# Optimization experiments

Hardware: AMD Instinct MI355X
Metric: run time of the kernel (lower is better)

## Reference

```python
import jax, jax.numpy as jnp
import numpy as np

B = 4096          # graphs in batch
NODES = 256       # nodes per graph
N = B * NODES     # total nodes
D = 64            # latent_dim
H = 128           # hidden
NEG = jnp.float32(np.finfo(np.float32).min)


def setup_inputs() -> dict:
    key = jax.random.key(0)
    ks = jax.random.split(key, 5)
    embed = jax.random.normal(ks[0], (N, D), jnp.float32)
    graph_embed = jax.random.normal(ks[1], (B, D), jnp.float32)
    prefix_sum = (jnp.arange(B, dtype=jnp.int32) + 1) * NODES  # cumulative node counts
    banned = jax.random.randint(ks[2], (N,), 0, 2) == 1        # per-node banned-action mask
    W1 = jax.random.normal(ks[3], (2 * D, H), jnp.float32) * 0.05
    b1 = jnp.zeros((H,), jnp.float32)
    W2 = jax.random.normal(ks[4], (H, 1), jnp.float32) * 0.05
    b2 = jnp.zeros((1,), jnp.float32)
    return dict(embed=embed, graph_embed=graph_embed, prefix_sum=prefix_sum,
                banned=banned, W1=W1, b1=b1, W2=W2, b2=b2)


def reference(embed, graph_embed, prefix_sum, banned, W1, b1, W2, b2):
    n = embed.shape[0]
    b = prefix_sum.shape[0]
    # node -> graph id (replaces rep_idx python loop in rep_global_embed)
    seg_ids = jnp.searchsorted(prefix_sum, jnp.arange(n, dtype=prefix_sum.dtype), side='right')
    g_rep = graph_embed[seg_ids]                                 # [N, D] gathered graph embed
    # linear_1 -> relu -> linear_out
    h = jax.nn.relu(jnp.concatenate([embed, g_rep], axis=1) @ W1 + b1)  # [N, H]
    raw_pred = h @ W2 + b2                                       # [N, 1]
    # greedy_actions: index_fill banned with float32 min, then per-graph argmax (jmax)
    q = jnp.where(banned, NEG, raw_pred[:, 0])                   # [N]
    seg_max = jax.ops.segment_max(q, seg_ids, num_segments=b)    # [B]
    is_max = q == seg_max[seg_ids]
    cand = jnp.where(is_max, jnp.arange(n), n)
    gidx = jax.ops.segment_min(cand, seg_ids, num_segments=b)    # global argmax per graph
    starts = jnp.concatenate([jnp.zeros((1,), prefix_sum.dtype), prefix_sum[:-1]])
    actions = gidx.astype(prefix_sum.dtype) - starts             # local (per-graph) action ids
    values = q[gidx]
    return actions, values, raw_pred
```

## Files before the change

kernel.cpp:

```cpp
#include <hip/hip_runtime.h>

#define NEGF (-3.402823466e+38f)
constexpr int BG = 4096;

typedef __attribute__((ext_vector_type(8))) short short8;
typedef __attribute__((ext_vector_type(4))) float f32x4;

constexpr int WT_STRIDE = 72;
constexpr int WT_ELEMS  = 128 * WT_STRIDE;

__device__ __forceinline__ void split_bf16(float a, short& hi, short& lo) {
    const unsigned u = __float_as_uint(a);
    hi = (short)(u >> 16);
    const float lof = a - __uint_as_float(u & 0xffff0000u);
    lo = (short)(__float_as_uint(lof) >> 16);
}

__global__ __launch_bounds__(256) void k_init(const float* __restrict__ W1,
                                              unsigned short* __restrict__ wt) {
    const int e = blockIdx.x * 256 + threadIdx.x;
    const int k = e >> 7, j = e & 127;
    short hi, lo;
    split_bf16(W1[e], hi, lo);
    wt[j * WT_STRIDE + k] = (unsigned short)hi;
    wt[WT_ELEMS + j * WT_STRIDE + k] = (unsigned short)lo;
}

__global__ __launch_bounds__(256, 2) void k_fused(
    const float* __restrict__ embed, const float* __restrict__ ge,
    const float* __restrict__ W1, const float* __restrict__ b1,
    const float* __restrict__ W2, const float* __restrict__ b2,
    const int* __restrict__ banned, const unsigned short* __restrict__ wt,
    float* __restrict__ out) {

    __shared__ __align__(16) unsigned short sW[2 * WT_ELEMS];
    __shared__ float s_ge[64];
    __shared__ float s_gp[2][128];
    __shared__ float s_gt[128];
    __shared__ float s_w2[128];
    __shared__ float s_raw[256];
    __shared__ float s_rv[4];
    __shared__ int   s_ri[4];

    const int t = threadIdx.x;
    const int lane = t & 63;
    const int w = t >> 6;
    const int quad = lane >> 4;
    const int l15 = lane & 15;
    const int g = blockIdx.x;

    const float* ebase = embed + ((size_t)g * 256 + (size_t)w * 64 + l15) * 64;
    f32x4 araw[4][2][2];
#pragma unroll
    for (int mt = 0; mt < 4; ++mt)
#pragma unroll
        for (int kc = 0; kc < 2; ++kc) {
            const float* p = ebase + mt * 1024 + kc * 32 + quad * 8;
            araw[mt][kc][0] = *(const f32x4*)p;
            araw[mt][kc][1] = *(const f32x4*)(p + 4);
        }

    {
        const uint4* src = (const uint4*)wt;
        uint4* dst = (uint4*)sW;
#pragma unroll
        for (int i = 0; i < 9; ++i) dst[i * 256 + t] = src[i * 256 + t];
    }
    if (t < 64) s_ge[t] = ge[g * 64 + t];
    if (t >= 64 && t < 192) s_w2[t - 64] = W2[t - 64];
    __syncthreads();

    {
        const int j = t & 127, h = t >> 7;
        float s = 0.f;
        const float* wb = W1 + (64 + h * 32) * 128 + j;
#pragma unroll
        for (int k = 0; k < 32; ++k) s = fmaf(s_ge[h * 32 + k], wb[k * 128], s);
        s_gp[h][j] = s;
    }
    __syncthreads();
    if (t < 128) s_gt[t] = s_gp[0][t] + s_gp[1][t] + b1[t];

    short8 ahi[4][2], alo[4][2];
#pragma unroll
    for (int mt = 0; mt < 4; ++mt)
#pragma unroll
        for (int kc = 0; kc < 2; ++kc)
#pragma unroll
            for (int i = 0; i < 8; ++i) {
                const float a = (i < 4) ? araw[mt][kc][0][i] : araw[mt][kc][1][i - 4];
                short hi, lo;
                split_bf16(a, hi, lo);
                ahi[mt][kc][i] = hi;
                alo[mt][kc][i] = lo;
            }

    f32x4 acc[4][8];
#pragma unroll
    for (int mt = 0; mt < 4; ++mt)
#pragma unroll
        for (int nt = 0; nt < 8; ++nt) acc[mt][nt] = f32x4{0.f, 0.f, 0.f, 0.f};

#pragma unroll
    for (int nt = 0; nt < 8; ++nt) {
        const unsigned short* rowp = sW + (nt * 16 + l15) * WT_STRIDE + quad * 8;
        const short8 bhi0 = *(const short8*)rowp;
        const short8 bhi1 = *(const short8*)(rowp + 32);
        const short8 blo0 = *(const short8*)(rowp + WT_ELEMS);
        const short8 blo1 = *(const short8*)(rowp + WT_ELEMS + 32);
#pragma unroll
        for (int mt = 0; mt < 4; ++mt) {
            f32x4 c = acc[mt][nt];
            c = __builtin_amdgcn_mfma_f32_16x16x32_bf16(ahi[mt][0], bhi0, c, 0, 0, 0);
            c = __builtin_amdgcn_mfma_f32_16x16x32_bf16(ahi[mt][1], bhi1, c, 0, 0, 0);
            c = __builtin_amdgcn_mfma_f32_16x16x32_bf16(alo[mt][0], bhi0, c, 0, 0, 0);
            c = __builtin_amdgcn_mfma_f32_16x16x32_bf16(alo[mt][1], bhi1, c, 0, 0, 0);
            c = __builtin_amdgcn_mfma_f32_16x16x32_bf16(ahi[mt][0], blo0, c, 0, 0, 0);
            c = __builtin_amdgcn_mfma_f32_16x16x32_bf16(ahi[mt][1], blo1, c, 0, 0, 0);
            acc[mt][nt] = c;
        }
    }

    __syncthreads();

    float gt8[8], w28[8];
#pragma unroll
    for (int nt = 0; nt < 8; ++nt) {
        gt8[nt] = s_gt[nt * 16 + l15];
        w28[nt] = s_w2[nt * 16 + l15];
    }
#pragma unroll
    for (int mt = 0; mt < 4; ++mt) {
        float pr[4] = {0.f, 0.f, 0.f, 0.f};
#pragma unroll
        for (int nt = 0; nt < 8; ++nt)
#pragma unroll
            for (int r = 0; r < 4; ++r)
                pr[r] = fmaf(fmaxf(acc[mt][nt][r] + gt8[nt], 0.f), w28[nt], pr[r]);
#pragma unroll
        for (int m = 1; m <= 8; m <<= 1)
#pragma unroll
            for (int r = 0; r < 4; ++r)
                pr[r] += __shfl_xor(pr[r], m, 64);
        if (l15 == 0) {
            float* dst = s_raw + w * 64 + mt * 16 + quad * 4;
            dst[0] = pr[0]; dst[1] = pr[1]; dst[2] = pr[2]; dst[3] = pr[3];
        }
    }
    __syncthreads();

    const float rp = s_raw[t] + b2[0];
    out[2 * BG + (size_t)g * 256 + t] = rp;
    float q = banned[(size_t)g * 256 + t] ? NEGF : rp;
    int idx = t;
#pragma unroll
    for (int off = 32; off >= 1; off >>= 1) {
        const float qv = __shfl_down(q, off, 64);
        const int iv = __shfl_down(idx, off, 64);
        if (qv > q || (qv == q && iv < idx)) { q = qv; idx = iv; }
    }
    if (lane == 0) { s_rv[w] = q; s_ri[w] = idx; }
    __syncthreads();
    if (t == 0) {
#pragma unroll
        for (int i = 1; i < 4; ++i)
            if (s_rv[i] > q || (s_rv[i] == q && s_ri[i] < idx)) { q = s_rv[i]; idx = s_ri[i]; }
        out[g] = (float)idx;
        out[BG + g] = q;
    }
}

extern "C" void kernel_launch(void* const* d_in, const int* in_sizes, int n_in,
                              void* d_out, int out_size, void* d_ws, size_t ws_size,
                              hipStream_t stream) {
    const float* embed  = (const float*)d_in[0];
    const float* gembed = (const float*)d_in[1];
    const int* banned   = (const int*)d_in[3];
    const float* W1     = (const float*)d_in[4];
    const float* b1     = (const float*)d_in[5];
    const float* W2     = (const float*)d_in[6];
    const float* b2     = (const float*)d_in[7];
    float* out = (float*)d_out;
    unsigned short* wt = (unsigned short*)d_ws;

    k_init<<<32, 256, 0, stream>>>(W1, wt);
    k_fused<<<BG, 256, 0, stream>>>(embed, gembed, W1, b1, W2, b2, banned, wt, out);
}
```

Measured before the change: 464.0 us.

## Split each graph over two blocks with precomputed graph term and atomic argmax

Moves the per-graph graph_embed·W1 projection into a separate kernel, then processes each graph with two 128-node blocks at higher occupancy. The per-graph argmax is combined across blocks with a 64-bit ordered-key atomicMax, and a final kernel decodes action and value. This aims to improve latency hiding and shrink per-block register pressure, but doubles the per-block weight copies into shared memory and adds two kernel launches plus a global round trip.

```diff
diff --git a/kernel.cpp b/kernel.cpp
--- a/kernel.cpp
+++ b/kernel.cpp
@@ -26,19 +26,31 @@
     wt[WT_ELEMS + j * WT_STRIDE + k] = (unsigned short)lo;
 }
 
-__global__ __launch_bounds__(256, 2) void k_fused(
-    const float* __restrict__ embed, const float* __restrict__ ge,
-    const float* __restrict__ W1, const float* __restrict__ b1,
-    const float* __restrict__ W2, const float* __restrict__ b2,
-    const int* __restrict__ banned, const unsigned short* __restrict__ wt,
-    float* __restrict__ out) {
+__global__ __launch_bounds__(128) void k_gterm(const float* __restrict__ ge,
+                                               const float* __restrict__ W1,
+                                               const float* __restrict__ b1,
+                                               float* __restrict__ gterm,
+                                               unsigned long long* __restrict__ keys) {
+    const int g = blockIdx.x, j = threadIdx.x;
+    if (j == 0) keys[g] = 0ull;
+    __shared__ float sg[64];
+    if (j < 64) sg[j] = ge[g * 64 + j];
+    __syncthreads();
+    float s = b1[j];
+    const float* w = W1 + 64 * 128 + j;
+#pragma unroll
+    for (int k = 0; k < 64; ++k) s = fmaf(sg[k], w[k * 128], s);
+    gterm[g * 128 + j] = s;
+}
+
+__global__ __launch_bounds__(256, 3) void k_main(
+    const float* __restrict__ embed, const float* __restrict__ gterm,
+    const unsigned short* __restrict__ wt, const float* __restrict__ W2,
+    const float* __restrict__ b2, const int* __restrict__ banned,
+    float* __restrict__ raw, unsigned long long* __restrict__ keys) {
 
     __shared__ __align__(16) unsigned short sW[2 * WT_ELEMS];
-    __shared__ float s_ge[64];
-    __shared__ float s_gp[2][128];
-    __shared__ float s_gt[128];
-    __shared__ float s_w2[128];
-    __shared__ float s_raw[256];
+    __shared__ float s_raw[128];
     __shared__ float s_rv[4];
     __shared__ int   s_ri[4];
 
@@ -47,18 +59,20 @@
     const int w = t >> 6;
     const int quad = lane >> 4;
     const int l15 = lane & 15;
-    const int g = blockIdx.x;
-
-    const float* ebase = embed + ((size_t)g * 256 + (size_t)w * 64 + l15) * 64;
-    f32x4 araw[4][2][2];
-#pragma unroll
-    for (int mt = 0; mt < 4; ++mt)
-#pragma unroll
-        for (int kc = 0; kc < 2; ++kc) {
-            const float* p = ebase + mt * 1024 + kc * 32 + quad * 8;
-            araw[mt][kc][0] = *(const f32x4*)p;
-            araw[mt][kc][1] = *(const f32x4*)(p + 4);
-        }
+    const int blk = blockIdx.x;
+    const int g = blk >> 1;
+    const int half = blk & 1;
+    const size_t node0 = (size_t)g * 256 + half * 128 + w * 32;
+
+    f32x4 araw[2][4];
+#pragma unroll
+    for (int mt = 0; mt < 2; ++mt) {
+        const float* p = embed + (node0 + mt * 16 + l15) * 64 + quad * 8;
+        araw[mt][0] = *(const f32x4*)p;
+        araw[mt][1] = *(const f32x4*)(p + 4);
+        araw[mt][2] = *(const f32x4*)(p + 32);
+        araw[mt][3] = *(const f32x4*)(p + 36);
+    }
 
     {
         const uint4* src = (const uint4*)wt;
@@ -66,38 +80,25 @@
 #pragma unroll
         for (int i = 0; i < 9; ++i) dst[i * 256 + t] = src[i * 256 + t];
     }
-    if (t < 64) s_ge[t] = ge[g * 64 + t];
-    if (t >= 64 && t < 192) s_w2[t - 64] = W2[t - 64];
-    __syncthreads();
-
-    {
-        const int j = t & 127, h = t >> 7;
-        float s = 0.f;
-        const float* wb = W1 + (64 + h * 32) * 128 + j;
-#pragma unroll
-        for (int k = 0; k < 32; ++k) s = fmaf(s_ge[h * 32 + k], wb[k * 128], s);
-        s_gp[h][j] = s;
-    }
-    __syncthreads();
-    if (t < 128) s_gt[t] = s_gp[0][t] + s_gp[1][t] + b1[t];
-
-    short8 ahi[4][2], alo[4][2];
-#pragma unroll
-    for (int mt = 0; mt < 4; ++mt)
+
+    short8 ahi[2][2], alo[2][2];
+#pragma unroll
+    for (int mt = 0; mt < 2; ++mt)
 #pragma unroll
         for (int kc = 0; kc < 2; ++kc)
 #pragma unroll
             for (int i = 0; i < 8; ++i) {
-                const float a = (i < 4) ? araw[mt][kc][0][i] : araw[mt][kc][1][i - 4];
+                const float a = (i < 4) ? araw[mt][kc * 2][i] : araw[mt][kc * 2 + 1][i - 4];
                 short hi, lo;
                 split_bf16(a, hi, lo);
                 ahi[mt][kc][i] = hi;
                 alo[mt][kc][i] = lo;
             }
-
-    f32x4 acc[4][8];
-#pragma unroll
-    for (int mt = 0; mt < 4; ++mt)
+    __syncthreads();
+
+    f32x4 acc[2][8];
+#pragma unroll
+    for (int mt = 0; mt < 2; ++mt)
 #pragma unroll
         for (int nt = 0; nt < 8; ++nt) acc[mt][nt] = f32x4{0.f, 0.f, 0.f, 0.f};
 
@@ -109,7 +110,7 @@
         const short8 blo0 = *(const short8*)(rowp + WT_ELEMS);
         const short8 blo1 = *(const short8*)(rowp + WT_ELEMS + 32);
 #pragma unroll
-        for (int mt = 0; mt < 4; ++mt) {
+        for (int mt = 0; mt < 2; ++mt) {
             f32x4 c = acc[mt][nt];
             c = __builtin_amdgcn_mfma_f32_16x16x32_bf16(ahi[mt][0], bhi0, c, 0, 0, 0);
             c = __builtin_amdgcn_mfma_f32_16x16x32_bf16(ahi[mt][1], bhi1, c, 0, 0, 0);
@@ -121,16 +122,15 @@
         }
     }
 
-    __syncthreads();
-
     float gt8[8], w28[8];
+    const float* gtp = gterm + g * 128;
 #pragma unroll
     for (int nt = 0; nt < 8; ++nt) {
-        gt8[nt] = s_gt[nt * 16 + l15];
-        w28[nt] = s_w2[nt * 16 + l15];
-    }
-#pragma unroll
-    for (int mt = 0; mt < 4; ++mt) {
+        gt8[nt] = gtp[nt * 16 + l15];
+        w28[nt] = W2[nt * 16 + l15];
+    }
+#pragma unroll
+    for (int mt = 0; mt < 2; ++mt) {
         float pr[4] = {0.f, 0.f, 0.f, 0.f};
 #pragma unroll
         for (int nt = 0; nt < 8; ++nt)
@@ -143,16 +143,19 @@
             for (int r = 0; r < 4; ++r)
                 pr[r] += __shfl_xor(pr[r], m, 64);
         if (l15 == 0) {
-            float* dst = s_raw + w * 64 + mt * 16 + quad * 4;
+            float* dst = s_raw + w * 32 + mt * 16 + quad * 4;
             dst[0] = pr[0]; dst[1] = pr[1]; dst[2] = pr[2]; dst[3] = pr[3];
         }
     }
     __syncthreads();
 
-    const float rp = s_raw[t] + b2[0];
-    out[2 * BG + (size_t)g * 256 + t] = rp;
-    float q = banned[(size_t)g * 256 + t] ? NEGF : rp;
+    float q = NEGF;
     int idx = t;
+    if (t < 128) {
+        const float rp = s_raw[t] + b2[0];
+        raw[(size_t)g * 256 + half * 128 + t] = rp;
+        q = banned[(size_t)g * 256 + half * 128 + t] ? NEGF : rp;
+    }
 #pragma unroll
     for (int off = 32; off >= 1; off >>= 1) {
         const float qv = __shfl_down(q, off, 64);
@@ -165,9 +168,27 @@
 #pragma unroll
         for (int i = 1; i < 4; ++i)
             if (s_rv[i] > q || (s_rv[i] == q && s_ri[i] < idx)) { q = s_rv[i]; idx = s_ri[i]; }
-        out[g] = (float)idx;
-        out[BG + g] = q;
-    }
+        const int lidx = half * 128 + idx;
+        const unsigned int fb = __float_as_uint(q);
+        const unsigned int ord = (fb & 0x80000000u) ? ~fb : (fb | 0x80000000u);
+        const unsigned long long key =
+            ((unsigned long long)ord << 32) | (unsigned int)(1023 - lidx);
+        atomicMax(&keys[g], key);
+    }
+}
+
+__global__ __launch_bounds__(256) void k_final(const unsigned long long* __restrict__ keys,
+                                               const float* __restrict__ raw,
+                                               const int* __restrict__ banned,
+                                               float* __restrict__ out) {
+    const int g = blockIdx.x * 256 + threadIdx.x;
+    if (g >= BG) return;
+    const unsigned long long key = keys[g];
+    const int lidx = 1023 - (int)(key & 0xFFFFFFFFull);
+    const int gi = g * 256 + lidx;
+    const float val = banned[gi] ? NEGF : raw[gi];
+    out[g] = (float)lidx;
+    out[BG + g] = val;
 }
 
 extern "C" void kernel_launch(void* const* d_in, const int* in_sizes, int n_in,
@@ -181,8 +202,14 @@
     const float* W2     = (const float*)d_in[6];
     const float* b2     = (const float*)d_in[7];
     float* out = (float*)d_out;
-    unsigned short* wt = (unsigned short*)d_ws;
+    float* raw = out + 2 * BG;
+
+    float* gterm = (float*)d_ws;
+    unsigned long long* keys = (unsigned long long*)((char*)d_ws + (size_t)BG * 128 * 4);
+    unsigned short* wt = (unsigned short*)((char*)keys + BG * 8);
 
     k_init<<<32, 256, 0, stream>>>(W1, wt);
-    k_fused<<<BG, 256, 0, stream>>>(embed, gembed, W1, b1, W2, b2, banned, wt, out);
-}
+    k_gterm<<<BG, 128, 0, stream>>>(gembed, W1, b1, gterm, keys);
+    k_main<<<2 * BG, 256, 0, stream>>>(embed, gterm, wt, W2, b2, banned, raw, keys);
+    k_final<<<(BG + 255) / 256, 256, 0, stream>>>(keys, raw, banned, out);
+}
```

Result: faster. 384.1 us (-17.2%).

## Split per-graph MLP into two half-tile passes to raise occupancy

Applied to the files above, without the earlier changes.

Each wave now processes its 64 rows as two passes of 32 rows instead of one pass of 64, halving the live accumulator and A-fragment registers so launch bounds can request 3 blocks per CU. The second half's embed loads are issued inside the loop, W2 is read directly from global instead of staged in shared memory, and the banned mask is loaded early. Lower register pressure is meant to give more latency hiding. The cost is less load/compute overlap within a block, possible spilling if the register target is not met, and more global W2 reads.

```diff
diff --git a/kernel.cpp b/kernel.cpp
--- a/kernel.cpp
+++ b/kernel.cpp
@@ -26,18 +26,17 @@
     wt[WT_ELEMS + j * WT_STRIDE + k] = (unsigned short)lo;
 }
 
-__global__ __launch_bounds__(256, 2) void k_fused(
+__global__ __launch_bounds__(256, 3) void k_main(
     const float* __restrict__ embed, const float* __restrict__ ge,
     const float* __restrict__ W1, const float* __restrict__ b1,
-    const float* __restrict__ W2, const float* __restrict__ b2,
-    const int* __restrict__ banned, const unsigned short* __restrict__ wt,
+    const unsigned short* __restrict__ wt, const float* __restrict__ W2,
+    const float* __restrict__ b2, const int* __restrict__ banned,
     float* __restrict__ out) {
 
     __shared__ __align__(16) unsigned short sW[2 * WT_ELEMS];
     __shared__ float s_ge[64];
     __shared__ float s_gp[2][128];
     __shared__ float s_gt[128];
-    __shared__ float s_w2[128];
     __shared__ float s_raw[256];
     __shared__ float s_rv[4];
     __shared__ int   s_ri[4];
@@ -49,16 +48,18 @@
     const int l15 = lane & 15;
     const int g = blockIdx.x;
 
-    const float* ebase = embed + ((size_t)g * 256 + (size_t)w * 64 + l15) * 64;
-    f32x4 araw[4][2][2];
-#pragma unroll
-    for (int mt = 0; mt < 4; ++mt)
-#pragma unroll
-        for (int kc = 0; kc < 2; ++kc) {
-            const float* p = ebase + mt * 1024 + kc * 32 + quad * 8;
-            araw[mt][kc][0] = *(const f32x4*)p;
-            araw[mt][kc][1] = *(const f32x4*)(p + 4);
-        }
+    const int bn = banned[(size_t)g * 256 + t];
+
+    const float* ebase0 = embed + ((size_t)g * 256 + w * 32 + l15) * 64 + quad * 8;
+    f32x4 araw[2][4];
+#pragma unroll
+    for (int mt = 0; mt < 2; ++mt) {
+        const float* p = ebase0 + mt * 16 * 64;
+        araw[mt][0] = *(const f32x4*)p;
+        araw[mt][1] = *(const f32x4*)(p + 4);
+        araw[mt][2] = *(const f32x4*)(p + 32);
+        araw[mt][3] = *(const f32x4*)(p + 36);
+    }
 
     {
         const uint4* src = (const uint4*)wt;
@@ -67,7 +68,6 @@
         for (int i = 0; i < 9; ++i) dst[i * 256 + t] = src[i * 256 + t];
     }
     if (t < 64) s_ge[t] = ge[g * 64 + t];
-    if (t >= 64 && t < 192) s_w2[t - 64] = W2[t - 64];
     __syncthreads();
 
     {
@@ -80,78 +80,91 @@
     }
     __syncthreads();
     if (t < 128) s_gt[t] = s_gp[0][t] + s_gp[1][t] + b1[t];
-
-    short8 ahi[4][2], alo[4][2];
-#pragma unroll
-    for (int mt = 0; mt < 4; ++mt)
-#pragma unroll
-        for (int kc = 0; kc < 2; ++kc)
-#pragma unroll
-            for (int i = 0; i < 8; ++i) {
-                const float a = (i < 4) ? araw[mt][kc][0][i] : araw[mt][kc][1][i - 4];
-                short hi, lo;
-                split_bf16(a, hi, lo);
-                ahi[mt][kc][i] = hi;
-                alo[mt][kc][i] = lo;
-            }
-
-    f32x4 acc[4][8];
-#pragma unroll
-    for (int mt = 0; mt < 4; ++mt)
-#pragma unroll
-        for (int nt = 0; nt < 8; ++nt) acc[mt][nt] = f32x4{0.f, 0.f, 0.f, 0.f};
-
-#pragma unroll
-    for (int nt = 0; nt < 8; ++nt) {
-        const unsigned short* rowp = sW + (nt * 16 + l15) * WT_STRIDE + quad * 8;
-        const short8 bhi0 = *(const short8*)rowp;
-        const short8 bhi1 = *(const short8*)(rowp + 32);
-        const short8 blo0 = *(const short8*)(rowp + WT_ELEMS);
-        const short8 blo1 = *(const short8*)(rowp + WT_ELEMS + 32);
-#pragma unroll
-        for (int mt = 0; mt < 4; ++mt) {
-            f32x4 c = acc[mt][nt];
-            c = __builtin_amdgcn_mfma_f32_16x16x32_bf16(ahi[mt][0], bhi0, c, 0, 0, 0);
-            c = __builtin_amdgcn_mfma_f32_16x16x32_bf16(ahi[mt][1], bhi1, c, 0, 0, 0);
-            c = __builtin_amdgcn_mfma_f32_16x16x32_bf16(alo[mt][0], bhi0, c, 0, 0, 0);
-            c = __builtin_amdgcn_mfma_f32_16x16x32_bf16(alo[mt][1], bhi1, c, 0, 0, 0);
-            c = __builtin_amdgcn_mfma_f32_16x16x32_bf16(ahi[mt][0], blo0, c, 0, 0, 0);
-            c = __builtin_amdgcn_mfma_f32_16x16x32_bf16(ahi[mt][1], blo1, c, 0, 0, 0);
-            acc[mt][nt] = c;
+    __syncthreads();
+
+    const float b2v = b2[0];
+
+#pragma unroll
+    for (int iter = 0; iter < 2; ++iter) {
+        if (iter == 1) {
+            const float* ebase = embed + ((size_t)g * 256 + 128 + w * 32 + l15) * 64 + quad * 8;
+#pragma unroll
+            for (int mt = 0; mt < 2; ++mt) {
+                const float* p = ebase + mt * 16 * 64;
+                araw[mt][0] = *(const f32x4*)p;
+                araw[mt][1] = *(const f32x4*)(p + 4);
+                araw[mt][2] = *(const f32x4*)(p + 32);
+                araw[mt][3] = *(const f32x4*)(p + 36);
+            }
         }
-    }
-
-    __syncthreads();
-
-    float gt8[8], w28[8];
-#pragma unroll
-    for (int nt = 0; nt < 8; ++nt) {
-        gt8[nt] = s_gt[nt * 16 + l15];
-        w28[nt] = s_w2[nt * 16 + l15];
-    }
-#pragma unroll
-    for (int mt = 0; mt < 4; ++mt) {
-        float pr[4] = {0.f, 0.f, 0.f, 0.f};
-#pragma unroll
-        for (int nt = 0; nt < 8; ++nt)
-#pragma unroll
-            for (int r = 0; r < 4; ++r)
-                pr[r] = fmaf(fmaxf(acc[mt][nt][r] + gt8[nt], 0.f), w28[nt], pr[r]);
-#pragma unroll
-        for (int m = 1; m <= 8; m <<= 1)
-#pragma unroll
-            for (int r = 0; r < 4; ++r)
-                pr[r] += __shfl_xor(pr[r], m, 64);
-        if (l15 == 0) {
-            float* dst = s_raw + w * 64 + mt * 16 + quad * 4;
-            dst[0] = pr[0]; dst[1] = pr[1]; dst[2] = pr[2]; dst[3] = pr[3];
+
+        short8 ahi[2][2], alo[2][2];
+#pragma unroll
+        for (int mt = 0; mt < 2; ++mt)
+#pragma unroll
+            for (int kc = 0; kc < 2; ++kc)
+#pragma unroll
+                for (int i = 0; i < 8; ++i) {
+                    const float a = (i < 4) ? araw[mt][kc * 2][i] : araw[mt][kc * 2 + 1][i - 4];
+                    short hi, lo;
+                    split_bf16(a, hi, lo);
+                    ahi[mt][kc][i] = hi;
+                    alo[mt][kc][i] = lo;
+                }
+
+        f32x4 acc[2][8];
+#pragma unroll
+        for (int mt = 0; mt < 2; ++mt)
+#pragma unroll
+            for (int nt = 0; nt < 8; ++nt) acc[mt][nt] = f32x4{0.f, 0.f, 0.f, 0.f};
+
+#pragma unroll
+        for (int nt = 0; nt < 8; ++nt) {
+            const unsigned short* rowp = sW + (nt * 16 + l15) * WT_STRIDE + quad * 8;
+            const short8 bhi0 = *(const short8*)rowp;
+            const short8 bhi1 = *(const short8*)(rowp + 32);
+            const short8 blo0 = *(const short8*)(rowp + WT_ELEMS);
+            const short8 blo1 = *(const short8*)(rowp + WT_ELEMS + 32);
+#pragma unroll
+            for (int mt = 0; mt < 2; ++mt) {
+                f32x4 c = acc[mt][nt];
+                c = __builtin_amdgcn_mfma_f32_16x16x32_bf16(ahi[mt][0], bhi0, c, 0, 0, 0);
+                c = __builtin_amdgcn_mfma_f32_16x16x32_bf16(ahi[mt][1], bhi1, c, 0, 0, 0);
+                c = __builtin_amdgcn_mfma_f32_16x16x32_bf16(alo[mt][0], bhi0, c, 0, 0, 0);
+                c = __builtin_amdgcn_mfma_f32_16x16x32_bf16(alo[mt][1], bhi1, c, 0, 0, 0);
+                c = __builtin_amdgcn_mfma_f32_16x16x32_bf16(ahi[mt][0], blo0, c, 0, 0, 0);
+                c = __builtin_amdgcn_mfma_f32_16x16x32_bf16(ahi[mt][1], blo1, c, 0, 0, 0);
+                acc[mt][nt] = c;
+            }
         }
-    }
-    __syncthreads();
-
-    const float rp = s_raw[t] + b2[0];
+
+#pragma unroll
+        for (int mt = 0; mt < 2; ++mt) {
+            float pr[4] = {0.f, 0.f, 0.f, 0.f};
+#pragma unroll
+            for (int nt = 0; nt < 8; ++nt) {
+                const float gt = s_gt[nt * 16 + l15];
+                const float w2 = W2[nt * 16 + l15];
+#pragma unroll
+                for (int r = 0; r < 4; ++r)
+                    pr[r] = fmaf(fmaxf(acc[mt][nt][r] + gt, 0.f), w2, pr[r]);
+            }
+#pragma unroll
+            for (int m = 1; m <= 8; m <<= 1)
+#pragma unroll
+                for (int r = 0; r < 4; ++r)
+                    pr[r] += __shfl_xor(pr[r], m, 64);
+            if (l15 == 0) {
+                float* dst = s_raw + iter * 128 + w * 32 + mt * 16 + quad * 4;
+                dst[0] = pr[0]; dst[1] = pr[1]; dst[2] = pr[2]; dst[3] = pr[3];
+            }
+        }
+    }
+    __syncthreads();
+
+    const float rp = s_raw[t] + b2v;
     out[2 * BG + (size_t)g * 256 + t] = rp;
-    float q = banned[(size_t)g * 256 + t] ? NEGF : rp;
+    float q = bn ? NEGF : rp;
     int idx = t;
 #pragma unroll
     for (int off = 32; off >= 1; off >>= 1) {
@@ -181,8 +194,9 @@
     const float* W2     = (const float*)d_in[6];
     const float* b2     = (const float*)d_in[7];
     float* out = (float*)d_out;
+
     unsigned short* wt = (unsigned short*)d_ws;
 
     k_init<<<32, 256, 0, stream>>>(W1, wt);
-    k_fused<<<BG, 256, 0, stream>>>(embed, gembed, W1, b1, W2, b2, banned, wt, out);
-}
+    k_main<<<BG, 256, 0, stream>>>(embed, gembed, W1, b1, wt, W2, b2, banned, out);
+}
```

After: 379.6 us. -18.2%, faster.
